# Performance work log

Measured on AMD Instinct MI355X. Metric: run time of the kernel, lower is better.

Reference implementation:

```python
import jax, jax.numpy as jnp
import numpy as np

B, T, D, DL, E, H, K = 4, 2048, 1024, 128, 8, 4, 3
HD = DL // H


def setup_inputs() -> dict:
    key = jax.random.key(0)
    ks = jax.random.split(key, 12)
    s = jnp.float32(0.02)
    f = lambda k, shape: jax.random.normal(k, shape, dtype=jnp.float32)
    zeros = lambda n: jnp.zeros((n,), jnp.float32)
    ones = lambda n: jnp.ones((n,), jnp.float32)
    return {
        "x": f(ks[0], (B, T, D)),
        "w_down": f(ks[1], (E * DL, D)) * s,
        "expert_pos_embed": f(ks[2], (1, E, DL)) * s,
        "global_proj_w": f(ks[3], (DL, D)) * s,
        "global_proj_b": zeros(DL),
        "attn_in_w": f(ks[4], (3 * DL, DL)) * s,
        "attn_in_b": zeros(3 * DL),
        "attn_out_w": f(ks[5], (DL, DL)) * s,
        "attn_out_b": zeros(DL),
        "norm_w": ones(DL),
        "norm_b": zeros(DL),
        "rq1_w": f(ks[6], (DL, DL)) * s,
        "rq1_b": zeros(DL),
        "rq_ln_w": ones(DL),
        "rq_ln_b": zeros(DL),
        "rq2_w": f(ks[7], (DL, DL)) * s,
        "rq2_b": zeros(DL),
        "rk_w": f(ks[8], (DL, DL)) * s,
        "rk_b": zeros(DL),
        "w_up": f(ks[9], (E, DL, D)) * s,
    }


def _ln(x, w, b):
    m = jnp.mean(x, axis=-1, keepdims=True)
    v = jnp.mean((x - m) ** 2, axis=-1, keepdims=True)
    return (x - m) * jax.lax.rsqrt(v + 1e-5) * w + b


def _gelu(x):
    return jax.nn.gelu(x, approximate=False)  # torch nn.GELU() default is exact erf


def reference(x, w_down, expert_pos_embed, global_proj_w, global_proj_b,
              attn_in_w, attn_in_b, attn_out_w, attn_out_b, norm_w, norm_b,
              rq1_w, rq1_b, rq_ln_w, rq_ln_b, rq2_w, rq2_b, rk_w, rk_b, w_up):
    N = B * T
    xf = x.reshape(N, D)
    expert_feats = (xf @ w_down.T).reshape(N, E, DL)  # [N,E,DL]
    # global context, broadcast to every token as a length-1 query
    gctx = x.mean(axis=1) @ global_proj_w.T + global_proj_b  # [B,DL]
    gctx = jnp.broadcast_to(gctx[:, None, :], (B, T, DL)).reshape(N, 1, DL)
    # 9-token (1 global + E experts) self-attention round table
    seq = jnp.concatenate([gctx, expert_feats + expert_pos_embed], axis=1)  # [N,E+1,DL]
    qkv = seq @ attn_in_w.T + attn_in_b
    q, k, v = jnp.split(qkv, 3, axis=-1)
    split_heads = lambda t: t.reshape(N, E + 1, H, HD).transpose(0, 2, 1, 3)
    q, k, v = split_heads(q), split_heads(k), split_heads(v)
    attn = jax.nn.softmax(jnp.einsum('nhqd,nhkd->nhqk', q, k) / jnp.sqrt(jnp.float32(HD)), axis=-1)
    o = jnp.einsum('nhqk,nhkd->nhqd', attn, v).transpose(0, 2, 1, 3).reshape(N, E + 1, DL)
    o = o @ attn_out_w.T + attn_out_b
    seq2 = _ln(o + seq, norm_w, norm_b)
    refined = seq2[:, 1:, :]  # [N,E,DL]
    # routing: refined expert keys vs projected global query
    rq = _gelu(_ln(gctx[:, 0, :] @ rq1_w.T + rq1_b, rq_ln_w, rq_ln_b)) @ rq2_w.T + rq2_b  # [N,DL]
    rk = refined @ rk_w.T + rk_b  # [N,E,DL]
    logits = jnp.einsum('nd,ned->ne', rq, rk) / jnp.sqrt(jnp.float32(DL))
    probs = jax.nn.softmax(logits, axis=-1)
    tw, ti = jax.lax.top_k(probs, K)
    tw = tw / tw.sum(axis=-1, keepdims=True)
    # expert up-projection; computing all E then gathering top-k outputs is
    # mathematically identical to gathering w_up[indices] first, but avoids
    # materializing the [N,K,DL,D] duplicated weight tensor
    all_out = jnp.einsum('ned,edm->nem', _gelu(expert_feats), w_up)  # [N,E,D]
    sel_out = jnp.take_along_axis(all_out, ti[:, :, None], axis=1)  # [N,K,D]
    weighted = jnp.sum(sel_out * tw[:, :, None], axis=1)  # [N,D]
    # aux load-balance loss
    mean_prob = probs.mean(axis=0)
    one_hot = jnp.zeros((N, E), probs.dtype).at[jnp.arange(N)[:, None], ti].set(1.0)
    mean_load = one_hot.mean(axis=0)
    aux_loss = E * jnp.sum(mean_prob * mean_load)
    return weighted.reshape(B, T, D), aux_loss
```

## Files before the change

### kernel.cpp

```cpp
#include <hip/hip_runtime.h>
#include <hip/hip_bf16.h>
#include <math.h>

#define BB 4
#define TT 2048
#define DD 1024
#define DLb 128
#define EE 8
#define HH 4
#define KK 3
#define HDh 32
#define NN (BB*TT)
#define NPOS 9
#define NCH 16
#define CHL (TT/NCH)
#define SEQSTR (NPOS*DLb)

typedef __attribute__((ext_vector_type(8))) short short8;
typedef __attribute__((ext_vector_type(4))) float f32x4;
typedef __attribute__((ext_vector_type(8))) unsigned short ushort8;
typedef __attribute__((ext_vector_type(4))) unsigned short ushort4v;

#define GLL(gptr, lptr) \
    __builtin_amdgcn_global_load_lds((const __attribute__((address_space(1))) unsigned int*)(gptr), \
                                     (__attribute__((address_space(3))) unsigned int*)(lptr), 16, 0, 0)

__device__ __forceinline__ float gelu_exact(float v) {
    return 0.5f * v * (1.0f + erff(v * 0.70710678118654752440f));
}

__device__ __forceinline__ unsigned short f2bf(float x) {
    __hip_bfloat16 h = __float2bfloat16(x);
    return *reinterpret_cast<unsigned short*>(&h);
}

__device__ __forceinline__ float bf2f(unsigned short u) {
    return __uint_as_float(((unsigned int)u) << 16);
}

__device__ __forceinline__ float4 rec4(const unsigned short* h, const unsigned short* l) {
    ushort4v hv = *(const ushort4v*)h;
    ushort4v lv = *(const ushort4v*)l;
    float4 r;
    r.x = bf2f(hv[0]) + bf2f(lv[0]);
    r.y = bf2f(hv[1]) + bf2f(lv[1]);
    r.z = bf2f(hv[2]) + bf2f(lv[2]);
    r.w = bf2f(hv[3]) + bf2f(lv[3]);
    return r;
}

__device__ __forceinline__ void stage512(const unsigned short* __restrict__ G,
                                         size_t rowBase, int L, int k0,
                                         unsigned short* lds, int tid)
{
    int r = tid >> 2;
    int sl = tid & 3;
    int src = sl ^ ((r >> 1) & 3);
    GLL(&G[(rowBase + r) * (size_t)L + k0 + src * 8], lds + (tid >> 6) * 512);
}

__device__ __forceinline__ int fragoff(int row, int fq) {
    return row * 32 + ((fq ^ ((row >> 1) & 3)) << 3);
}

__global__ __launch_bounds__(256) void ksplit(const float* __restrict__ src,
                                              unsigned short* __restrict__ h,
                                              unsigned short* __restrict__ l, int n8)
{
    int i = blockIdx.x * 256 + threadIdx.x;
    if (i >= n8) return;
    size_t g = (size_t)i * 8;
    float4 a = *(const float4*)&src[g];
    float4 b = *(const float4*)&src[g + 4];
    float vv[8] = {a.x, a.y, a.z, a.w, b.x, b.y, b.z, b.w};
    ushort8 ho, lo;
    #pragma unroll
    for (int j = 0; j < 8; j++) {
        unsigned short hh = f2bf(vv[j]);
        float hf = bf2f(hh);
        ho[j] = hh;
        lo[j] = f2bf(vv[j] - hf);
    }
    *(ushort8*)&h[g] = ho;
    *(ushort8*)&l[g] = lo;
}

__global__ __launch_bounds__(256) void k1a(const float* __restrict__ x, float* __restrict__ partial,
                                           unsigned short* __restrict__ xh,
                                           unsigned short* __restrict__ xl) {
    int d = blockIdx.x * 256 + threadIdx.x;
    int b = blockIdx.y, c = blockIdx.z;
    size_t base = ((size_t)b * TT + (size_t)c * CHL) * DD + d;
    float s = 0.0f;
    for (int t = 0; t < CHL; t++) {
        size_t idx = base + (size_t)t * DD;
        float v = x[idx];
        s += v;
        unsigned short h = f2bf(v);
        xh[idx] = h;
        xl[idx] = f2bf(v - bf2f(h));
    }
    partial[(b * NCH + c) * DD + d] = s;
}

__global__ __launch_bounds__(256) void k1b(const float* __restrict__ partial, float* __restrict__ mean_x) {
    int d = blockIdx.x * 256 + threadIdx.x;
    int b = blockIdx.y;
    float s = 0.0f;
    for (int c = 0; c < NCH; c++) s += partial[(b * NCH + c) * DD + d];
    mean_x[b * DD + d] = s * (1.0f / TT);
}

__global__ __launch_bounds__(128) void k2_batch(
    const float* __restrict__ mean_x,
    const float* __restrict__ gpw, const float* __restrict__ gpb,
    const float* __restrict__ rq1w, const float* __restrict__ rq1b,
    const float* __restrict__ lnw, const float* __restrict__ lnb,
    const float* __restrict__ rq2w, const float* __restrict__ rq2b,
    const float* __restrict__ rkw, const float* __restrict__ rkb,
    float* __restrict__ gctx, float* __restrict__ uv, float* __restrict__ c0v)
{
    int b = blockIdx.x, d = threadIdx.x;
    __shared__ __attribute__((aligned(16))) float g[DLb];
    __shared__ __attribute__((aligned(16))) float t1[DLb];
    __shared__ __attribute__((aligned(16))) float act[DLb];
    __shared__ __attribute__((aligned(16))) float rqs[DLb];
    __shared__ float red[2];
    {
        const float4* wrow = (const float4*)(gpw + (size_t)d * DD);
        const float4* mx4  = (const float4*)(mean_x + (size_t)b * DD);
        float s = gpb[d];
        for (int k = 0; k < DD / 4; k++) {
            float4 w = wrow[k], m = mx4[k];
            s += w.x * m.x + w.y * m.y + w.z * m.z + w.w * m.w;
        }
        g[d] = s;
        gctx[b * DLb + d] = s;
    }
    __syncthreads();
    {
        float s = rq1b[d];
        for (int k = 0; k < DLb; k++) s += g[k] * rq1w[d * DLb + k];
        t1[d] = s;
    }
    __syncthreads();
    if (d == 0) {
        float m = 0.0f;
        for (int i = 0; i < DLb; i++) m += t1[i];
        m *= (1.0f / DLb);
        float v = 0.0f;
        for (int i = 0; i < DLb; i++) { float df = t1[i] - m; v += df * df; }
        v *= (1.0f / DLb);
        red[0] = m; red[1] = 1.0f / sqrtf(v + 1e-5f);
    }
    __syncthreads();
    {
        float xn = (t1[d] - red[0]) * red[1] * lnw[d] + lnb[d];
        act[d] = gelu_exact(xn);
    }
    __syncthreads();
    {
        float s = rq2b[d];
        for (int k = 0; k < DLb; k++) s += act[k] * rq2w[d * DLb + k];
        rqs[d] = s;
    }
    __syncthreads();
    {
        float u = 0.0f;
        for (int k = 0; k < DLb; k++) u += rqs[k] * rkw[(size_t)k * DLb + d];
        uv[b * DLb + d] = u;
    }
    if (d == 0) {
        float c0 = 0.0f;
        for (int k = 0; k < DLb; k++) c0 += rqs[k] * rkb[k];
        c0v[b] = c0;
    }
}

__global__ __launch_bounds__(256) void k2b(const float* __restrict__ gctx,
                                           unsigned short* __restrict__ seqh,
                                           unsigned short* __restrict__ seql) {
    int i = blockIdx.x * 256 + threadIdx.x;
    int n = i >> 7, d = i & 127;
    float v = gctx[(n >> 11) * DLb + d];
    unsigned short h = f2bf(v);
    seqh[(size_t)n * SEQSTR + d] = h;
    seql[(size_t)n * SEQSTR + d] = f2bf(v - bf2f(h));
}

__global__ __launch_bounds__(512, 4) void k3s(const unsigned short* __restrict__ XH,
                                              const unsigned short* __restrict__ XL,
                                              const unsigned short* __restrict__ WH,
                                              const unsigned short* __restrict__ WL,
                                              const float* __restrict__ pe,
                                              unsigned short* __restrict__ seqh,
                                              unsigned short* __restrict__ seql)
{
    __shared__ __attribute__((aligned(16))) unsigned short Ah[2][128 * 32];
    __shared__ __attribute__((aligned(16))) unsigned short Al[2][128 * 32];
    __shared__ __attribute__((aligned(16))) unsigned short Bh[2][128 * 32];
    __shared__ __attribute__((aligned(16))) unsigned short Bl[2][128 * 32];
    int tid = threadIdx.x;
    int lane = tid & 63, wave = tid >> 6;
    int wm = wave & 1, wn = wave >> 1;
    int b = blockIdx.y * 8 + blockIdx.x;
    int nbid = (b & 7) * 64 + (b >> 3);
    int row0 = (nbid >> 3) * 128, col0 = (nbid & 7) * 128;
    int fr = lane & 15, fq = lane >> 4;
    f32x4 acc[4][2];
    #pragma unroll
    for (int i = 0; i < 4; i++)
        #pragma unroll
        for (int j = 0; j < 2; j++) acc[i][j] = (f32x4)0.0f;

    for (int k0 = 0; k0 < DD; k0 += 64) {
        stage512(XH, row0, DD, k0,      Ah[0], tid);
        stage512(XH, row0, DD, k0 + 32, Ah[1], tid);
        stage512(XL, row0, DD, k0,      Al[0], tid);
        stage512(XL, row0, DD, k0 + 32, Al[1], tid);
        stage512(WH, col0, DD, k0,      Bh[0], tid);
        stage512(WH, col0, DD, k0 + 32, Bh[1], tid);
        stage512(WL, col0, DD, k0,      Bl[0], tid);
        stage512(WL, col0, DD, k0 + 32, Bl[1], tid);
        __syncthreads();
        #pragma unroll
        for (int ks = 0; ks < 2; ks++) {
            short8 ah[4], al4[4], bh[2], bl4[2];
            #pragma unroll
            for (int f = 0; f < 4; f++) {
                int ra = fragoff(wm * 64 + f * 16 + fr, fq);
                ah[f]  = *(const short8*)&Ah[ks][ra];
                al4[f] = *(const short8*)&Al[ks][ra];
            }
            #pragma unroll
            for (int g = 0; g < 2; g++) {
                int rb = fragoff(wn * 32 + g * 16 + fr, fq);
                bh[g]  = *(const short8*)&Bh[ks][rb];
                bl4[g] = *(const short8*)&Bl[ks][rb];
            }
            #pragma unroll
            for (int i = 0; i < 4; i++)
                #pragma unroll
                for (int j = 0; j < 2; j++) {
                    acc[i][j] = __builtin_amdgcn_mfma_f32_16x16x32_bf16(ah[i],  bh[j],  acc[i][j], 0, 0, 0);
                    acc[i][j] = __builtin_amdgcn_mfma_f32_16x16x32_bf16(ah[i],  bl4[j], acc[i][j], 0, 0, 0);
                    acc[i][j] = __builtin_amdgcn_mfma_f32_16x16x32_bf16(al4[i], bh[j],  acc[i][j], 0, 0, 0);
                }
        }
        __syncthreads();
    }
    #pragma unroll
    for (int j = 0; j < 2; j++) {
        int gc = col0 + wn * 32 + j * 16 + fr;
        float pv = pe[gc];
        #pragma unroll
        for (int i = 0; i < 4; i++) {
            #pragma unroll
            for (int r = 0; r < 4; r++) {
                int gr = row0 + wm * 64 + i * 16 + fq * 4 + r;
                float v = acc[i][j][r] + pv;
                unsigned short h = f2bf(v);
                size_t idx = (size_t)gr * SEQSTR + DLb + gc;
                seqh[idx] = h;
                seql[idx] = f2bf(v - bf2f(h));
            }
        }
    }
}

__global__ __launch_bounds__(512, 2) void k4f(const unsigned short* __restrict__ SH,
                                              const unsigned short* __restrict__ SL,
                                              const unsigned short* __restrict__ WHp,
                                              const unsigned short* __restrict__ WLp,
                                              const float* __restrict__ bias,
                                              float* __restrict__ og)
{
    __shared__ __attribute__((aligned(16))) float smemf[40512];
    float* qbuf  = smemf;
    float* kbuf  = smemf + 128 * 132;
    float* attnw = smemf + 128 * 132 + 144 * 132;
    float* vbuf  = smemf;
    unsigned short* Ah = (unsigned short*)smemf;
    unsigned short* Al = (unsigned short*)(smemf + 2304);

    int tid = threadIdx.x;
    int lane = tid & 63, w = tid >> 6;
    int fr = lane & 15, fq = lane >> 4;
    int colBase = w * 48;
    size_t rowBase = (size_t)blockIdx.x * 144;

    f32x4 acc[9][3];
    #pragma unroll
    for (int i = 0; i < 9; i++)
        #pragma unroll
        for (int g = 0; g < 3; g++) acc[i][g] = (f32x4)0.0f;

    for (int k0 = 0; k0 < DLb; k0 += 32) {
        {
            int r = tid >> 2, sl = tid & 3;
            int src = sl ^ ((r >> 1) & 3);
            GLL(&SH[(rowBase + r) * (size_t)DLb + k0 + src * 8], Ah + w * 512);
            GLL(&SL[(rowBase + r) * (size_t)DLb + k0 + src * 8], Al + w * 512);
            if (tid < 64) {
                int r2 = 128 + (tid >> 2);
                int src2 = (tid & 3) ^ ((r2 >> 1) & 3);
                GLL(&SH[(rowBase + r2) * (size_t)DLb + k0 + src2 * 8], Ah + 4096);
                GLL(&SL[(rowBase + r2) * (size_t)DLb + k0 + src2 * 8], Al + 4096);
            }
        }
        __syncthreads();
        short8 bh[3], bl[3];
        #pragma unroll
        for (int g = 0; g < 3; g++) {
            int col = colBase + g * 16 + fr;
            bh[g] = *(const short8*)&WHp[(size_t)col * DLb + k0 + fq * 8];
            bl[g] = *(const short8*)&WLp[(size_t)col * DLb + k0 + fq * 8];
        }
        #pragma unroll
        for (int i = 0; i < 9; i++) {
            int ra = fragoff(i * 16 + fr, fq);
            short8 ah  = *(const short8*)&Ah[ra];
            short8 al4 = *(const short8*)&Al[ra];
            #pragma unroll
            for (int g = 0; g < 3; g++) {
                acc[i][g] = __builtin_amdgcn_mfma_f32_16x16x32_bf16(ah,  bh[g], acc[i][g], 0, 0, 0);
                acc[i][g] = __builtin_amdgcn_mfma_f32_16x16x32_bf16(ah,  bl[g], acc[i][g], 0, 0, 0);
                acc[i][g] = __builtin_amdgcn_mfma_f32_16x16x32_bf16(al4, bh[g], acc[i][g], 0, 0, 0);
            }
        }
        __syncthreads();
    }

    #pragma unroll
    for (int g = 0; g < 3; g++) {
        int cg = colBase + g * 16;
        if (cg < 256) {
            float bv = bias[cg + fr];
            #pragma unroll
            for (int i = 0; i < 9; i++) {
                #pragma unroll
                for (int rr = 0; rr < 4; rr++) {
                    int lr = i * 16 + fq * 4 + rr;
                    float v = acc[i][g][rr] + bv;
                    if (cg < 128) {
                        int t = lr / 9, p = lr - t * 9;
                        if (p) qbuf[(t * 8 + p - 1) * 132 + cg + fr] = v;
                    } else {
                        kbuf[lr * 132 + (cg - 128) + fr] = v;
                    }
                }
            }
        }
    }
    __syncthreads();

    {
        int t = tid >> 5, h = (tid >> 3) & 3, ii = 1 + (tid & 7);
        const float* qrow = &qbuf[(t * 8 + ii - 1) * 132 + h * HDh];
        float4 q4[8];
        #pragma unroll
        for (int q = 0; q < 8; q++) q4[q] = *(const float4*)&qrow[q * 4];
        float sc[NPOS];
        float mx = -1e30f;
        for (int j = 0; j < NPOS; j++) {
            const float* krow = &kbuf[(t * 9 + j) * 132 + h * HDh];
            float s = 0.0f;
            #pragma unroll
            for (int q = 0; q < 8; q++) {
                float4 k4 = *(const float4*)&krow[q * 4];
                s += q4[q].x * k4.x;
                s += q4[q].y * k4.y;
                s += q4[q].z * k4.z;
                s += q4[q].w * k4.w;
            }
            s *= 0.17677669529663687f;
            sc[j] = s;
            mx = fmaxf(mx, s);
        }
        float se = 0.0f;
        for (int j = 0; j < NPOS; j++) { sc[j] = expf(sc[j] - mx); se += sc[j]; }
        float inv = 1.0f / se;
        for (int j = 0; j < NPOS; j++) attnw[((t * 4 + h) * 8 + (ii - 1)) * 9 + j] = sc[j] * inv;
    }
    __syncthreads();

    #pragma unroll
    for (int g = 0; g < 3; g++) {
        int cg = colBase + g * 16;
        if (cg >= 256) {
            float bv = bias[cg + fr];
            #pragma unroll
            for (int i = 0; i < 9; i++) {
                #pragma unroll
                for (int rr = 0; rr < 4; rr++) {
                    int lr = i * 16 + fq * 4 + rr;
                    vbuf[lr * 132 + (cg - 256) + fr] = acc[i][g][rr] + bv;
                }
            }
        }
    }
    __syncthreads();

    {
        int dq = tid & 31, rb = tid >> 5;
        int h = dq >> 3;
        #pragma unroll
        for (int k = 0; k < 8; k++) {
            int orow = rb + 16 * k;
            int t = orow >> 3, pm1 = orow & 7;
            const float* aw = &attnw[((t * 4 + h) * 8 + pm1) * 9];
            float4 s; s.x = 0.0f; s.y = 0.0f; s.z = 0.0f; s.w = 0.0f;
            #pragma unroll
            for (int j = 0; j < NPOS; j++) {
                float a = aw[j];
                float4 v4 = *(const float4*)&vbuf[(t * 9 + j) * 132 + dq * 4];
                s.x += a * v4.x; s.y += a * v4.y; s.z += a * v4.z; s.w += a * v4.w;
            }
            *(float4*)&og[((size_t)(blockIdx.x * 16 + t) * 8 + pm1) * DLb + dq * 4] = s;
        }
    }
}

__global__ __launch_bounds__(256) void k4cd(const float* __restrict__ A,
                                            const float* __restrict__ W,
                                            const float* __restrict__ bias,
                                            const unsigned short* __restrict__ seqh,
                                            const unsigned short* __restrict__ seql,
                                            const float* __restrict__ nw,
                                            const float* __restrict__ nb,
                                            const float* __restrict__ uv,
                                            const float* __restrict__ c0v,
                                            float* __restrict__ logits)
{
    __shared__ __attribute__((aligned(16))) float As[16][132];
    __shared__ __attribute__((aligned(16))) float Bs[16][132];
    __shared__ float redS[128][17];
    __shared__ float mstat[128][2];
    int tid = threadIdx.x;
    int tx = tid & 15, ty = tid >> 4;
    int row0 = blockIdx.y * 128;
    float acc[8][8] = {};
    for (int k0 = 0; k0 < DLb; k0 += 16) {
        #pragma unroll
        for (int i = 0; i < 2; i++) {
            int L = i * 256 + tid;
            int r = L >> 2, kq = (L & 3) * 4;
            float4 a4 = *(const float4*)&A[(size_t)(row0 + r) * DLb + k0 + kq];
            float4 b4 = *(const float4*)&W[(size_t)r * DLb + k0 + kq];
            As[kq + 0][r] = a4.x; As[kq + 1][r] = a4.y; As[kq + 2][r] = a4.z; As[kq + 3][r] = a4.w;
            Bs[kq + 0][r] = b4.x; Bs[kq + 1][r] = b4.y; Bs[kq + 2][r] = b4.z; Bs[kq + 3][r] = b4.w;
        }
        __syncthreads();
        #pragma unroll
        for (int kk = 0; kk < 16; kk++) {
            float4 a0 = *(const float4*)&As[kk][ty * 4];
            float4 a1 = *(const float4*)&As[kk][64 + ty * 4];
            float4 b0 = *(const float4*)&Bs[kk][tx * 4];
            float4 b1 = *(const float4*)&Bs[kk][64 + tx * 4];
            float ar[8] = {a0.x, a0.y, a0.z, a0.w, a1.x, a1.y, a1.z, a1.w};
            float bc[8] = {b0.x, b0.y, b0.z, b0.w, b1.x, b1.y, b1.z, b1.w};
            #pragma unroll
            for (int i = 0; i < 8; i++)
                #pragma unroll
                for (int j = 0; j < 8; j++)
                    acc[i][j] += ar[i] * bc[j];
        }
        __syncthreads();
    }
    int b = row0 >> 14;
    float4 bb0 = *(const float4*)&bias[tx * 4];
    float4 bb1 = *(const float4*)&bias[64 + tx * 4];
    #pragma unroll
    for (int i = 0; i < 8; i++) {
        int rl = (i < 4) ? (ty * 4 + i) : (64 + ty * 4 + (i - 4));
        int m = row0 + rl;
        size_t roff = (size_t)(m >> 3) * SEQSTR + (size_t)((m & 7) + 1) * DLb;
        float4 r0 = rec4(&seqh[roff + tx * 4], &seql[roff + tx * 4]);
        float4 r1 = rec4(&seqh[roff + 64 + tx * 4], &seql[roff + 64 + tx * 4]);
        acc[i][0] += bb0.x + r0.x; acc[i][1] += bb0.y + r0.y;
        acc[i][2] += bb0.z + r0.z; acc[i][3] += bb0.w + r0.w;
        acc[i][4] += bb1.x + r1.x; acc[i][5] += bb1.y + r1.y;
        acc[i][6] += bb1.z + r1.z; acc[i][7] += bb1.w + r1.w;
        float ps = 0.0f;
        #pragma unroll
        for (int j = 0; j < 8; j++) ps += acc[i][j];
        redS[rl][tx] = ps;
    }
    __syncthreads();
    if (tid < 128) {
        float s = 0.0f;
        #pragma unroll
        for (int t = 0; t < 16; t++) s += redS[tid][t];
        mstat[tid][0] = s * (1.0f / DLb);
    }
    __syncthreads();
    #pragma unroll
    for (int i = 0; i < 8; i++) {
        int rl = (i < 4) ? (ty * 4 + i) : (64 + ty * 4 + (i - 4));
        float m = mstat[rl][0];
        float pv = 0.0f;
        #pragma unroll
        for (int j = 0; j < 8; j++) { float df = acc[i][j] - m; pv += df * df; }
        redS[rl][tx] = pv;
    }
    __syncthreads();
    if (tid < 128) {
        float s = 0.0f;
        #pragma unroll
        for (int t = 0; t < 16; t++) s += redS[tid][t];
        mstat[tid][1] = 1.0f / sqrtf(s * (1.0f / DLb) + 1e-5f);
    }
    __syncthreads();
    const float* u = uv + b * DLb;
    float4 nw0 = *(const float4*)&nw[tx * 4];
    float4 nw1 = *(const float4*)&nw[64 + tx * 4];
    float4 nb0 = *(const float4*)&nb[tx * 4];
    float4 nb1 = *(const float4*)&nb[64 + tx * 4];
    float4 u0 = *(const float4*)&u[tx * 4];
    float4 u1 = *(const float4*)&u[64 + tx * 4];
    #pragma unroll
    for (int i = 0; i < 8; i++) {
        int rl = (i < 4) ? (ty * 4 + i) : (64 + ty * 4 + (i - 4));
        float m = mstat[rl][0], istd = mstat[rl][1];
        float ps;
        ps  = ((acc[i][0] - m) * istd * nw0.x + nb0.x) * u0.x;
        ps += ((acc[i][1] - m) * istd * nw0.y + nb0.y) * u0.y;
        ps += ((acc[i][2] - m) * istd * nw0.z + nb0.z) * u0.z;
        ps += ((acc[i][3] - m) * istd * nw0.w + nb0.w) * u0.w;
        ps += ((acc[i][4] - m) * istd * nw1.x + nb1.x) * u1.x;
        ps += ((acc[i][5] - m) * istd * nw1.y + nb1.y) * u1.y;
        ps += ((acc[i][6] - m) * istd * nw1.z + nb1.z) * u1.z;
        ps += ((acc[i][7] - m) * istd * nw1.w + nb1.w) * u1.w;
        redS[rl][tx] = ps;
    }
    __syncthreads();
    if (tid < 128) {
        float s = 0.0f;
        #pragma unroll
        for (int t = 0; t < 16; t++) s += redS[tid][t];
        logits[row0 + tid] = (s + c0v[b]) * 0.08838834764831845f;
    }
}

__global__ __launch_bounds__(256) void k4e(const float* __restrict__ logits,
                                           float* __restrict__ probs,
                                           float* __restrict__ wsel)
{
    int n = blockIdx.x * 256 + threadIdx.x;
    if (n >= NN) return;
    float lg[EE];
    float4 l0 = *(const float4*)&logits[(size_t)n * EE];
    float4 l1 = *(const float4*)&logits[(size_t)n * EE + 4];
    lg[0] = l0.x; lg[1] = l0.y; lg[2] = l0.z; lg[3] = l0.w;
    lg[4] = l1.x; lg[5] = l1.y; lg[6] = l1.z; lg[7] = l1.w;
    float mx = lg[0];
    #pragma unroll
    for (int e = 1; e < EE; e++) mx = fmaxf(mx, lg[e]);
    float pr[EE];
    float se = 0.0f;
    #pragma unroll
    for (int e = 0; e < EE; e++) { pr[e] = expf(lg[e] - mx); se += pr[e]; }
    float inv = 1.0f / se;
    #pragma unroll
    for (int e = 0; e < EE; e++) pr[e] *= inv;
    float4 p0, p1;
    p0.x = pr[0]; p0.y = pr[1]; p0.z = pr[2]; p0.w = pr[3];
    p1.x = pr[4]; p1.y = pr[5]; p1.z = pr[6]; p1.w = pr[7];
    *(float4*)&probs[(size_t)n * EE] = p0;
    *(float4*)&probs[(size_t)n * EE + 4] = p1;
    bool used[EE] = {};
    int sel[KK];
    float sw = 0.0f;
    for (int t = 0; t < KK; t++) {
        int bi = 0; float bv = -1e30f;
        for (int e = 0; e < EE; e++)
            if (!used[e] && pr[e] > bv) { bv = pr[e]; bi = e; }
        used[bi] = true; sel[t] = bi; sw += pr[bi];
    }
    float invsw = 1.0f / sw;
    float w8[EE];
    #pragma unroll
    for (int e = 0; e < EE; e++) w8[e] = 0.0f;
    for (int t = 0; t < KK; t++) w8[sel[t]] = pr[sel[t]] * invsw;
    float4 w0, w1;
    w0.x = w8[0]; w0.y = w8[1]; w0.z = w8[2]; w0.w = w8[3];
    w1.x = w8[4]; w1.y = w8[5]; w1.z = w8[6]; w1.w = w8[7];
    *(float4*)&wsel[(size_t)n * EE] = w0;
    *(float4*)&wsel[(size_t)n * EE + 4] = w1;
}

__global__ __launch_bounds__(256) void k5pre(const unsigned short* __restrict__ seqh,
                                             const unsigned short* __restrict__ seql,
                                             const float* __restrict__ pe,
                                             const float* __restrict__ wsel,
                                             unsigned short* __restrict__ abf)
{
    size_t g = ((size_t)blockIdx.x * 256 + threadIdx.x) * 8;
    int n = (int)(g >> 10), k0 = (int)(g & 1023);
    int e = k0 >> 7;
    float w = wsel[(size_t)n * EE + e];
    size_t soff = (size_t)n * SEQSTR + DLb + k0;
    ushort8 hv = *(const ushort8*)&seqh[soff];
    ushort8 lv = *(const ushort8*)&seql[soff];
    float4 p0 = *(const float4*)&pe[k0];
    float4 p1 = *(const float4*)&pe[k0 + 4];
    float pp[8] = {p0.x, p0.y, p0.z, p0.w, p1.x, p1.y, p1.z, p1.w};
    ushort8 o;
    #pragma unroll
    for (int i = 0; i < 8; i++) {
        float v = bf2f(hv[i]) + bf2f(lv[i]) - pp[i];
        o[i] = f2bf(w * gelu_exact(v));
    }
    *(ushort8*)&abf[g] = o;
}

__global__ __launch_bounds__(256) void k5t(const float* __restrict__ wup, unsigned short* __restrict__ wupT) {
    __shared__ float T[64][68];
    int tid = threadIdx.x;
    int k0 = blockIdx.x * 64, m0 = blockIdx.y * 64;
    #pragma unroll
    for (int i = 0; i < 4; i++) {
        int F = i * 256 + tid;
        int r = F >> 4, c4 = (F & 15) * 4;
        *(float4*)&T[r][c4] = *(const float4*)&wup[(size_t)(k0 + r) * DD + m0 + c4];
    }
    __syncthreads();
    #pragma unroll
    for (int i = 0; i < 2; i++) {
        int W = i * 256 + tid;
        int r = W >> 3, c8 = (W & 7) * 8;
        ushort8 o;
        #pragma unroll
        for (int j = 0; j < 8; j++) o[j] = f2bf(T[c8 + j][r]);
        *(ushort8*)&wupT[(size_t)(m0 + r) * DD + k0 + c8] = o;
    }
}

__global__ __launch_bounds__(512, 6) void k5_mfma(const unsigned short* __restrict__ A,
                                                  const unsigned short* __restrict__ B,
                                                  float* __restrict__ C)
{
    __shared__ __attribute__((aligned(16))) unsigned short As[2][128 * 32];
    __shared__ __attribute__((aligned(16))) unsigned short Bs[2][128 * 32];
    int tid = threadIdx.x;
    int lane = tid & 63, wave = tid >> 6;
    int wm = wave & 1, wn = wave >> 1;
    int b = blockIdx.y * 8 + blockIdx.x;
    int nbid = (b & 7) * 64 + (b >> 3);
    int row0 = (nbid >> 3) * 128, col0 = (nbid & 7) * 128;
    int fr = lane & 15, fq = lane >> 4;
    f32x4 acc[4][2];
    #pragma unroll
    for (int i = 0; i < 4; i++)
        #pragma unroll
        for (int j = 0; j < 2; j++) acc[i][j] = (f32x4)0.0f;

    for (int k0 = 0; k0 < DD; k0 += 64) {
        stage512(A, row0, DD, k0,      As[0], tid);
        stage512(A, row0, DD, k0 + 32, As[1], tid);
        stage512(B, col0, DD, k0,      Bs[0], tid);
        stage512(B, col0, DD, k0 + 32, Bs[1], tid);
        __syncthreads();
        #pragma unroll
        for (int ks = 0; ks < 2; ks++) {
            short8 af[4], bf[2];
            #pragma unroll
            for (int f = 0; f < 4; f++)
                af[f] = *(const short8*)&As[ks][fragoff(wm * 64 + f * 16 + fr, fq)];
            #pragma unroll
            for (int g = 0; g < 2; g++)
                bf[g] = *(const short8*)&Bs[ks][fragoff(wn * 32 + g * 16 + fr, fq)];
            #pragma unroll
            for (int i = 0; i < 4; i++)
                #pragma unroll
                for (int j = 0; j < 2; j++)
                    acc[i][j] = __builtin_amdgcn_mfma_f32_16x16x32_bf16(af[i], bf[j], acc[i][j], 0, 0, 0);
        }
        __syncthreads();
    }
    #pragma unroll
    for (int i = 0; i < 4; i++) {
        #pragma unroll
        for (int j = 0; j < 2; j++) {
            int gc = col0 + wn * 32 + j * 16 + fr;
            #pragma unroll
            for (int r = 0; r < 4; r++) {
                int gr = row0 + wm * 64 + i * 16 + fq * 4 + r;
                C[(size_t)gr * DD + gc] = acc[i][j][r];
            }
        }
    }
}

__global__ __launch_bounds__(256) void k6a(const float* __restrict__ probs,
                                           const float* __restrict__ wsel,
                                           float* __restrict__ part)
{
    int tid = threadIdx.x;
    int n = blockIdx.x * 256 + tid;
    float lp[EE], lc[EE];
    #pragma unroll
    for (int e = 0; e < EE; e++) {
        lp[e] = probs[(size_t)n * EE + e];
        lc[e] = (wsel[(size_t)n * EE + e] > 0.0f) ? 1.0f : 0.0f;
    }
    __shared__ float bp[256][EE];
    __shared__ float bc[256][EE];
    #pragma unroll
    for (int e = 0; e < EE; e++) { bp[tid][e] = lp[e]; bc[tid][e] = lc[e]; }
    __syncthreads();
    for (int s = 128; s > 0; s >>= 1) {
        if (tid < s) {
            #pragma unroll
            for (int e = 0; e < EE; e++) {
                bp[tid][e] += bp[tid + s][e];
                bc[tid][e] += bc[tid + s][e];
            }
        }
        __syncthreads();
    }
    if (tid < EE) {
        part[blockIdx.x * 16 + tid] = bp[0][tid];
        part[blockIdx.x * 16 + 8 + tid] = bc[0][tid];
    }
}

__global__ __launch_bounds__(64) void k6b(const float* __restrict__ part, float* __restrict__ out_aux) {
    int tid = threadIdx.x;
    __shared__ float sums[16];
    if (tid < 16) {
        float s = 0.0f;
        for (int b = 0; b < NN / 256; b++) s += part[b * 16 + tid];
        sums[tid] = s;
    }
    __syncthreads();
    if (tid == 0) {
        float a = 0.0f;
        for (int e = 0; e < EE; e++) a += (sums[e] / NN) * (sums[8 + e] / NN);
        out_aux[0] = EE * a;
    }
}

extern "C" void kernel_launch(void* const* d_in, const int* in_sizes, int n_in,
                              void* d_out, int out_size, void* d_ws, size_t ws_size,
                              hipStream_t stream) {
    const float* x     = (const float*)d_in[0];
    const float* wdown = (const float*)d_in[1];
    const float* pe    = (const float*)d_in[2];
    const float* gpw   = (const float*)d_in[3];
    const float* gpb   = (const float*)d_in[4];
    const float* aiw   = (const float*)d_in[5];
    const float* aib   = (const float*)d_in[6];
    const float* aow   = (const float*)d_in[7];
    const float* aob   = (const float*)d_in[8];
    const float* nw    = (const float*)d_in[9];
    const float* nb    = (const float*)d_in[10];
    const float* rq1w  = (const float*)d_in[11];
    const float* rq1b  = (const float*)d_in[12];
    const float* rqlnw = (const float*)d_in[13];
    const float* rqlnb = (const float*)d_in[14];
    const float* rq2w  = (const float*)d_in[15];
    const float* rq2b  = (const float*)d_in[16];
    const float* rkw   = (const float*)d_in[17];
    const float* rkb   = (const float*)d_in[18];
    const float* wup   = (const float*)d_in[19];

    float* out = (float*)d_out;

    unsigned short* seqh = (unsigned short*)d_ws;
    unsigned short* seql = seqh + (size_t)NN * SEQSTR;
    float* xregion = (float*)(seql + (size_t)NN * SEQSTR);
    unsigned short* xh = (unsigned short*)xregion;
    unsigned short* xl = xh + (size_t)NN * DD;
    float* o = xregion;
    unsigned short* abf = (unsigned short*)xregion;
    float* region = xregion + (size_t)NN * DD;
    float* probs  = region + (size_t)65536 * 128;
    float* wsel   = probs + (size_t)NN * EE;
    float* logits = wsel + (size_t)NN * EE;
    float* partial= logits + (size_t)NN * EE;
    float* mean_x = partial + (size_t)BB * NCH * DD;
    float* gctx   = mean_x + (size_t)BB * DD;
    float* uv     = gctx + (size_t)BB * DLb;
    float* c0v    = uv + (size_t)BB * DLb;
    float* k6part = c0v + 64;
    unsigned short* wupT = (unsigned short*)(k6part + 512);
    unsigned short* wdh  = wupT + (size_t)DD * DD;
    unsigned short* wdl  = wdh + (size_t)DD * DD;
    unsigned short* aiwh = wdl + (size_t)DD * DD;
    unsigned short* aiwl = aiwh + (size_t)384 * DLb;

    hipLaunchKernelGGL(ksplit, dim3(DD * DD / 8 / 256), dim3(256), 0, stream, wdown, wdh, wdl, DD * DD / 8);
    hipLaunchKernelGGL(ksplit, dim3(384 * DLb / 8 / 256), dim3(256), 0, stream, aiw, aiwh, aiwl, 384 * DLb / 8);

    hipLaunchKernelGGL(k1a, dim3(DD / 256, BB, NCH), dim3(256), 0, stream, x, partial, xh, xl);
    hipLaunchKernelGGL(k1b, dim3(DD / 256, BB), dim3(256), 0, stream, partial, mean_x);
    hipLaunchKernelGGL(k2_batch, dim3(BB), dim3(DLb), 0, stream,
                       mean_x, gpw, gpb, rq1w, rq1b, rqlnw, rqlnb, rq2w, rq2b, rkw, rkb,
                       gctx, uv, c0v);
    hipLaunchKernelGGL(k2b, dim3(NN * DLb / 256), dim3(256), 0, stream, gctx, seqh, seql);
    hipLaunchKernelGGL(k3s, dim3((EE * DLb) / 128, NN / 128), dim3(512), 0, stream,
                       xh, xl, wdh, wdl, pe, seqh, seql);
    hipLaunchKernelGGL(k4f, dim3(NN / 16), dim3(512), 0, stream,
                       seqh, seql, aiwh, aiwl, aib, o);
    hipLaunchKernelGGL(k4cd, dim3(1, NN * EE / 128), dim3(256), 0, stream,
                       o, aow, aob, seqh, seql, nw, nb, uv, c0v, logits);
    hipLaunchKernelGGL(k4e, dim3(NN / 256), dim3(256), 0, stream, logits, probs, wsel);
    hipLaunchKernelGGL(k5t, dim3(DD / 64, DD / 64), dim3(256), 0, stream, wup, wupT);
    hipLaunchKernelGGL(k5pre, dim3(NN * DD / (256 * 8)), dim3(256), 0, stream, seqh, seql, pe, wsel, abf);
    hipLaunchKernelGGL(k5_mfma, dim3(DD / 128, NN / 128), dim3(512), 0, stream, abf, wupT, out);
    hipLaunchKernelGGL(k6a, dim3(NN / 256), dim3(256), 0, stream, probs, wsel, k6part);
    hipLaunchKernelGGL(k6b, dim3(1), dim3(64), 0, stream, k6part, out + (size_t)NN * DD);
}
```

Measured before the change: 358.3 us.

## Shrink k4f shared memory by processing attention heads in two passes, keep weights in registers

The fused QKV+attention kernel now stages Q and K for only two heads at a time in a 68-stride buffer, running the score/softmax in two passes, and keeps each thread's attention weights in registers instead of an LDS attnw array. This cuts the shared-memory footprint from about 162KB to about 76KB, and launch bounds are raised to request 4 blocks per CU. The price is extra barriers, half the threads idling in each score pass, and tighter register pressure from the 27 MFMA accumulators under the higher occupancy target, which could cause spills. The PV step is also reorganised so each thread writes 32 contiguous output values for its own head.

New measurement: 473.4 us. +32.1%, slower.

```diff
diff --git a/kernel.cpp b/kernel.cpp
--- a/kernel.cpp
+++ b/kernel.cpp
@@ -268,18 +268,16 @@
     }
 }
 
-__global__ __launch_bounds__(512, 2) void k4f(const unsigned short* __restrict__ SH,
+__global__ __launch_bounds__(512, 4) void k4f(const unsigned short* __restrict__ SH,
                                               const unsigned short* __restrict__ SL,
                                               const unsigned short* __restrict__ WHp,
                                               const unsigned short* __restrict__ WLp,
                                               const float* __restrict__ bias,
                                               float* __restrict__ og)
 {
-    __shared__ __attribute__((aligned(16))) float smemf[40512];
-    float* qbuf  = smemf;
-    float* kbuf  = smemf + 128 * 132;
-    float* attnw = smemf + 128 * 132 + 144 * 132;
-    float* vbuf  = smemf;
+    __shared__ __attribute__((aligned(16))) float smemf[19008];
+    float* qk   = smemf;
+    float* vbuf = smemf;
     unsigned short* Ah = (unsigned short*)smemf;
     unsigned short* Al = (unsigned short*)(smemf + 2304);
 
@@ -331,58 +329,71 @@
         __syncthreads();
     }
 
-    #pragma unroll
-    for (int g = 0; g < 3; g++) {
-        int cg = colBase + g * 16;
-        if (cg < 256) {
-            float bv = bias[cg + fr];
-            #pragma unroll
-            for (int i = 0; i < 9; i++) {
+    int st  = (tid & 255) >> 4;
+    int sh2 = (tid >> 3) & 1;
+    int sii = 1 + (tid & 7);
+    int shp = tid >> 8;
+    float aw[NPOS];
+
+    for (int hp = 0; hp < 2; hp++) {
+        #pragma unroll
+        for (int g = 0; g < 3; g++) {
+            int cg = colBase + g * 16;
+            int cq = cg - hp * 64;
+            int ck = cg - 128 - hp * 64;
+            if (cq >= 0 && cq < 64) {
+                float bv = bias[cg + fr];
                 #pragma unroll
-                for (int rr = 0; rr < 4; rr++) {
-                    int lr = i * 16 + fq * 4 + rr;
-                    float v = acc[i][g][rr] + bv;
-                    if (cg < 128) {
+                for (int i = 0; i < 9; i++) {
+                    #pragma unroll
+                    for (int rr = 0; rr < 4; rr++) {
+                        int lr = i * 16 + fq * 4 + rr;
                         int t = lr / 9, p = lr - t * 9;
-                        if (p) qbuf[(t * 8 + p - 1) * 132 + cg + fr] = v;
-                    } else {
-                        kbuf[lr * 132 + (cg - 128) + fr] = v;
+                        if (p) qk[(t * 8 + p - 1) * 68 + cq + fr] = acc[i][g][rr] + bv;
                     }
                 }
-            }
-        }
-    }
-    __syncthreads();
-
-    {
-        int t = tid >> 5, h = (tid >> 3) & 3, ii = 1 + (tid & 7);
-        const float* qrow = &qbuf[(t * 8 + ii - 1) * 132 + h * HDh];
-        float4 q4[8];
-        #pragma unroll
-        for (int q = 0; q < 8; q++) q4[q] = *(const float4*)&qrow[q * 4];
-        float sc[NPOS];
-        float mx = -1e30f;
-        for (int j = 0; j < NPOS; j++) {
-            const float* krow = &kbuf[(t * 9 + j) * 132 + h * HDh];
-            float s = 0.0f;
-            #pragma unroll
-            for (int q = 0; q < 8; q++) {
-                float4 k4 = *(const float4*)&krow[q * 4];
-                s += q4[q].x * k4.x;
-                s += q4[q].y * k4.y;
-                s += q4[q].z * k4.z;
-                s += q4[q].w * k4.w;
-            }
-            s *= 0.17677669529663687f;
-            sc[j] = s;
-            mx = fmaxf(mx, s);
-        }
-        float se = 0.0f;
-        for (int j = 0; j < NPOS; j++) { sc[j] = expf(sc[j] - mx); se += sc[j]; }
-        float inv = 1.0f / se;
-        for (int j = 0; j < NPOS; j++) attnw[((t * 4 + h) * 8 + (ii - 1)) * 9 + j] = sc[j] * inv;
-    }
-    __syncthreads();
+            } else if (ck >= 0 && ck < 64) {
+                float bv = bias[cg + fr];
+                #pragma unroll
+                for (int i = 0; i < 9; i++) {
+                    #pragma unroll
+                    for (int rr = 0; rr < 4; rr++) {
+                        int lr = i * 16 + fq * 4 + rr;
+                        qk[(128 + lr) * 68 + ck + fr] = acc[i][g][rr] + bv;
+                    }
+                }
+            }
+        }
+        __syncthreads();
+        if (shp == hp) {
+            const float* qrow = &qk[(st * 8 + sii - 1) * 68 + sh2 * 32];
+            float4 q4[8];
+            #pragma unroll
+            for (int q = 0; q < 8; q++) q4[q] = *(const float4*)&qrow[q * 4];
+            float sc[NPOS];
+            float mx = -1e30f;
+            for (int j = 0; j < NPOS; j++) {
+                const float* krow = &qk[(128 + st * 9 + j) * 68 + sh2 * 32];
+                float s = 0.0f;
+                #pragma unroll
+                for (int q = 0; q < 8; q++) {
+                    float4 k4 = *(const float4*)&krow[q * 4];
+                    s += q4[q].x * k4.x;
+                    s += q4[q].y * k4.y;
+                    s += q4[q].z * k4.z;
+                    s += q4[q].w * k4.w;
+                }
+                s *= 0.17677669529663687f;
+                sc[j] = s;
+                mx = fmaxf(mx, s);
+            }
+            float se = 0.0f;
+            for (int j = 0; j < NPOS; j++) { sc[j] = expf(sc[j] - mx); se += sc[j]; }
+            float inv = 1.0f / se;
+            for (int j = 0; j < NPOS; j++) aw[j] = sc[j] * inv;
+        }
+        __syncthreads();
+    }
 
     #pragma unroll
     for (int g = 0; g < 3; g++) {
@@ -402,22 +413,23 @@
     __syncthreads();
 
     {
-        int dq = tid & 31, rb = tid >> 5;
-        int h = dq >> 3;
-        #pragma unroll
-        for (int k = 0; k < 8; k++) {
-            int orow = rb + 16 * k;
-            int t = orow >> 3, pm1 = orow & 7;
-            const float* aw = &attnw[((t * 4 + h) * 8 + pm1) * 9];
-            float4 s; s.x = 0.0f; s.y = 0.0f; s.z = 0.0f; s.w = 0.0f;
-            #pragma unroll
-            for (int j = 0; j < NPOS; j++) {
-                float a = aw[j];
-                float4 v4 = *(const float4*)&vbuf[(t * 9 + j) * 132 + dq * 4];
-                s.x += a * v4.x; s.y += a * v4.y; s.z += a * v4.z; s.w += a * v4.w;
-            }
-            *(float4*)&og[((size_t)(blockIdx.x * 16 + t) * 8 + pm1) * DLb + dq * 4] = s;
-        }
+        int sh = shp * 2 + sh2;
+        float4 s[8];
+        #pragma unroll
+        for (int q = 0; q < 8; q++) { s[q].x = 0.0f; s[q].y = 0.0f; s[q].z = 0.0f; s[q].w = 0.0f; }
+        for (int j = 0; j < NPOS; j++) {
+            float a = aw[j];
+            const float* vrow = &vbuf[(st * 9 + j) * 132 + sh * 32];
+            #pragma unroll
+            for (int q = 0; q < 8; q++) {
+                float4 v4 = *(const float4*)&vrow[q * 4];
+                s[q].x += a * v4.x; s[q].y += a * v4.y;
+                s[q].z += a * v4.z; s[q].w += a * v4.w;
+            }
+        }
+        float* orow = &og[((size_t)(blockIdx.x * 16 + st) * 8 + (sii - 1)) * DLb + sh * 32];
+        #pragma unroll
+        for (int q = 0; q < 8; q++) *(float4*)&orow[q * 4] = s[q];
     }
 }
 
```
